# Optimization experiments

Hardware: AMD Instinct MI355X
Metric: run time of the kernel (lower is better)

## Reference

```python
import jax, jax.numpy as jnp
import numpy as np

B, N, K = 32, 511, 2          # trees per batch, nodes per tree (full binary), max children
IN_DIM, MEM_DIM = 256, 256


def _build_children_idx():
    # Heap tree (node p has children 2p+1, 2p+2), relabeled i -> N-1-i so that every
    # child id < parent id; then a single pass i = 0..N-1 is a valid topological order
    # (leaves first, root last at index N-1). Padded child slots are -1.
    ch = np.full((N, K), -1, dtype=np.int64)
    for p in range(N):
        for k in range(K):
            c = 2 * p + 1 + k
            if c < N:
                ch[N - 1 - p, k] = N - 1 - c
    return jnp.asarray(ch)


def setup_inputs() -> dict:
    key = jax.random.key(0)
    ks = jax.random.split(key, 9)
    s_in = float(1.0 / np.sqrt(IN_DIM))   # torch Linear default init bound
    s_m = float(1.0 / np.sqrt(MEM_DIM))
    u = lambda k, shape, s: jax.random.uniform(k, shape, jnp.float32, -s, s)
    return {
        "inputs": jax.random.normal(ks[0], (B, N, IN_DIM), jnp.float32),
        "W_ioux": u(ks[1], (3 * MEM_DIM, IN_DIM), s_in),
        "b_ioux": u(ks[2], (3 * MEM_DIM,), s_in),
        "W_iouh": u(ks[3], (3 * MEM_DIM, MEM_DIM), s_m),
        "b_iouh": u(ks[4], (3 * MEM_DIM,), s_m),
        "W_fx": u(ks[5], (MEM_DIM, IN_DIM), s_in),
        "b_fx": u(ks[6], (MEM_DIM,), s_in),
        "W_fh": u(ks[7], (MEM_DIM, MEM_DIM), s_m),
        "b_fh": u(ks[8], (MEM_DIM,), s_m),
        "children_idx": _build_children_idx(),
    }


def reference(inputs, W_ioux, b_ioux, W_iouh, b_iouh, W_fx, b_fx, W_fh, b_fh,
              children_idx):
    # Input-only projections depend on no recurrent state -> one big GEMM up front.
    x_iou = jnp.einsum('bni,oi->nbo', inputs, W_ioux) + b_ioux   # [N,B,3M]
    x_f = jnp.einsum('bni,mi->nbm', inputs, W_fx) + b_fx          # [N,B,M]

    def step(carry, xs):
        c_buf, h_buf, idx = carry                  # [N,B,M], [N,B,M], scalar node id
        ch, xi, xf = xs                            # [K], [B,3M], [B,M]
        valid = ch >= 0
        mask = valid.astype(c_buf.dtype)[:, None, None]
        safe = jnp.where(valid, ch, 0)
        child_c = c_buf[safe] * mask               # [K,B,M] (zeros for padded / leaf)
        child_h = h_buf[safe] * mask               # [K,B,M]
        h_sum = child_h.sum(0)                     # [B,M]  (child-sum)
        iou = xi + h_sum @ W_iouh.T + b_iouh       # [B,3M]
        i, o, u = jnp.split(iou, 3, axis=-1)
        i, o, u = jax.nn.sigmoid(i), jax.nn.sigmoid(o), jnp.tanh(u)
        # per-child forget gate: fh(child_h) + fx(inputs) broadcast over children
        f = jax.nn.sigmoid(jnp.einsum('kbm,nm->kbn', child_h, W_fh) + b_fh + xf[None])
        c = i * u + (f * child_c).sum(0)           # [B,M]
        h = o * jnp.tanh(c)
        c_buf = c_buf.at[idx].set(c)
        h_buf = h_buf.at[idx].set(h)
        return (c_buf, h_buf, idx + 1), None

    zeros = jnp.zeros((N, B, MEM_DIM), inputs.dtype)
    (c_buf, h_buf, _), _ = jax.lax.scan(
        step, (zeros, zeros, jnp.int32(0)), (children_idx, x_iou, x_f))

    root_c = c_buf[N - 1]                # [B,M]
    root_h = h_buf[N - 1]                # [B,M]
    hiddens = h_buf.transpose(1, 0, 2)   # [B,N,M]: h of node i at row i (tree.idx == i)
    return root_c, root_h, hiddens
```

## Files before the change

kernel.cpp:

```cpp
#include <hip/hip_runtime.h>
#include <hip/hip_bf16.h>


#define NN 511
#define BB 32
#define DD 256

typedef __attribute__((ext_vector_type(8))) short short8;
typedef __attribute__((ext_vector_type(4))) short short4v;
typedef __attribute__((ext_vector_type(4))) float f32x4;

#define MFMA __builtin_amdgcn_mfma_f32_16x16x32_bf16

#define OFF_XBF   0UL
#define OFF_HBF   8372224UL
#define OFF_CBUF  16744448UL
#define OFF_PART  33488896UL
#define OFF_WX    66912256UL
#define OFF_WH    67436544UL
#define OFF_BIAS  67960832UL

__device__ __forceinline__ short f2bf(float f) {
    union { float f; unsigned int u; } v; v.f = f;
    unsigned int r = (v.u + 0x7FFFu + ((v.u >> 16) & 1u)) >> 16;
    return (short)(unsigned short)r;
}
__device__ __forceinline__ float sigmf(float x) { return 1.0f / (1.0f + __expf(-x)); }
__device__ __forceinline__ float tanhc(float x) {
    x = fminf(fmaxf(x, -15.f), 15.f);
    float e = __expf(2.f * x);
    return (e - 1.f) / (e + 1.f);
}

__global__ void prep_x(const float* __restrict__ inp, short* __restrict__ xbf) {
    int idx = blockIdx.x * 256 + threadIdx.x;
    if (idx >= NN * BB * 64) return;
    int n = idx / (BB * 64);
    int rem = idx - n * (BB * 64);
    int b = rem >> 6;
    int c4 = rem & 63;
    float4 v = ((const float4*)(inp + ((long)b * NN + n) * DD))[c4];
    short4v sv = { f2bf(v.x), f2bf(v.y), f2bf(v.z), f2bf(v.w) };
    *(short4v*)(xbf + (long)idx * 4) = sv;
}

__global__ void prep_w(const float* __restrict__ Wix, const float* __restrict__ Wih,
                       const float* __restrict__ Wfx, const float* __restrict__ Wfh,
                       const float* __restrict__ bix, const float* __restrict__ bih,
                       const float* __restrict__ bfx, const float* __restrict__ bfh,
                       short* __restrict__ wx, short* __restrict__ wh,
                       float* __restrict__ bias) {
    int tid = blockIdx.x * 256 + threadIdx.x;
    if (tid >= 1024 * 256) return;
    int row = tid >> 8, c = tid & 255;
    float vx = (row < 768) ? Wix[row * 256 + c] : Wfx[(row - 768) * 256 + c];
    float vh = (row < 768) ? Wih[row * 256 + c] : Wfh[(row - 768) * 256 + c];
    wx[tid] = f2bf(vx);
    wh[tid] = f2bf(vh);
    if (c == 0)
        bias[row] = (row < 768) ? (bix[row] + bih[row]) : (bfx[row - 768] + bfh[row - 768]);
}

__device__ __forceinline__ void stage_w(const short* __restrict__ wsrc, int mt,
                                        short* __restrict__ lb, int tid) {
#pragma unroll
    for (int it = 0; it < 8; ++it) {
        const int u = it * 256 + tid;
        const int s = u >> 9;
        const int r = (u >> 5) & 15;
        const int c8 = u & 31;
        const int k = c8 * 8;
        short8 v = *(const short8*)(wsrc + ((long)(s * 256 + mt * 16 + r) * 256 + k));
        *(short8*)(lb + (s * 16 + r) * 256 + (k ^ ((r & 7) << 3))) = v;
    }
}

__global__ __launch_bounds__(256, 4) void xproj(
    const short* __restrict__ xbf, const short* __restrict__ wx,
    const float* __restrict__ bias, short* __restrict__ hbf,
    float* __restrict__ cbuf, float* __restrict__ part, float* __restrict__ out) {
    __shared__ short lb[4 * 16 * 256];
    const int tid = threadIdx.x;
    const int mt = blockIdx.y;
    stage_w(wx, mt, lb, tid);
    __syncthreads();

    const int lane = tid & 63;
    const int wid = tid >> 6;
    const int rt = blockIdx.x * 4 + wid;
    if (rt >= 2 * NN) return;
    const int arow = lane & 15;
    const int kgrp = lane >> 4;
    const int node = rt >> 1;
    const int bh = rt & 1;
    const int m = mt * 16 + arow;
    const int swz = (arow & 7) << 3;

    const short* ap = xbf + ((long)rt * 16 + arow) * DD + kgrp * 8;
    short8 a[8];
#pragma unroll
    for (int ks = 0; ks < 8; ++ks) a[ks] = *(const short8*)(ap + ks * 32);

    f32x4 ai = {0.f, 0.f, 0.f, 0.f}, ao = ai, au = ai, af = ai;
    const short* b0 = lb + (0 * 16 + arow) * 256;
    const short* b1 = lb + (1 * 16 + arow) * 256;
    const short* b2 = lb + (2 * 16 + arow) * 256;
    const short* b3 = lb + (3 * 16 + arow) * 256;
#pragma unroll
    for (int ks = 0; ks < 8; ++ks) {
        const int ko = (ks * 32 + kgrp * 8) ^ swz;
        short8 wi = *(const short8*)(b0 + ko);
        short8 wo = *(const short8*)(b1 + ko);
        short8 wu = *(const short8*)(b2 + ko);
        short8 wf = *(const short8*)(b3 + ko);
        ai = MFMA(a[ks], wi, ai, 0, 0, 0);
        ao = MFMA(a[ks], wo, ao, 0, 0, 0);
        au = MFMA(a[ks], wu, au, 0, 0, 0);
        af = MFMA(a[ks], wf, af, 0, 0, 0);
    }

    if (node < 256) {
        const float bi = bias[m], bo = bias[256 + m], bu = bias[512 + m];
#pragma unroll
        for (int r = 0; r < 4; ++r) {
            const int b = bh * 16 + kgrp * 4 + r;
            const float iv = sigmf(ai[r] + bi);
            const float ov = sigmf(ao[r] + bo);
            const float uv = tanhc(au[r] + bu);
            const float c = iv * uv;
            const float h = ov * tanhc(c);
            const long rowg = (long)node * BB + b;
            cbuf[rowg * DD + m] = c;
            hbf[rowg * DD + m] = f2bf(h);
            out[2 * BB * DD + ((long)b * NN + node) * DD + m] = h;
        }
    } else {
        const float bi = bias[m], bo = bias[256 + m], bu = bias[512 + m], bf = bias[768 + m];
#pragma unroll
        for (int r = 0; r < 4; ++r) {
            const int b = bh * 16 + kgrp * 4 + r;
            const long prow = ((long)(node - 256) * BB + b) * 1024;
            part[prow + m] = ai[r] + bi;
            part[prow + 256 + m] = ao[r] + bo;
            part[prow + 512 + m] = au[r] + bu;
            part[prow + 768 + m] = af[r] + bf;
        }
    }
}

__global__ __launch_bounds__(256, 4) void level_h(
    const short* __restrict__ wh, short* __restrict__ hbf,
    float* __restrict__ cbuf, const float* __restrict__ part,
    float* __restrict__ out, int istart, int ncount) {
    __shared__ short lb[4 * 16 * 256];
    const int tid = threadIdx.x;
    const int mt = blockIdx.y;
    stage_w(wh, mt, lb, tid);
    __syncthreads();

    const int lane = tid & 63;
    const int wid = tid >> 6;
    const int rt = blockIdx.x * 4 + wid;
    if (rt >= ncount * 2) return;
    const int arow = lane & 15;
    const int kgrp = lane >> 4;
    const int node = istart + (rt >> 1);
    const int bh = rt & 1;
    const int m = mt * 16 + arow;
    const int swz = (arow & 7) << 3;
    const int c0 = 2 * node - 511, c1 = 2 * node - 512;

    const short* ap0 = hbf + ((long)c0 * BB + bh * 16 + arow) * DD + kgrp * 8;
    const short* ap1 = hbf + ((long)c1 * BB + bh * 16 + arow) * DD + kgrp * 8;
    short8 a0[8], a1[8];
#pragma unroll
    for (int ks = 0; ks < 8; ++ks) {
        a0[ks] = *(const short8*)(ap0 + ks * 32);
        a1[ks] = *(const short8*)(ap1 + ks * 32);
    }

    f32x4 ai = {0.f, 0.f, 0.f, 0.f}, ao = ai, au = ai, f0a = ai, f1a = ai;
    const short* b0 = lb + (0 * 16 + arow) * 256;
    const short* b1 = lb + (1 * 16 + arow) * 256;
    const short* b2 = lb + (2 * 16 + arow) * 256;
    const short* b3 = lb + (3 * 16 + arow) * 256;
#pragma unroll
    for (int ks = 0; ks < 8; ++ks) {
        const int ko = (ks * 32 + kgrp * 8) ^ swz;
        short8 wi = *(const short8*)(b0 + ko);
        short8 wo = *(const short8*)(b1 + ko);
        short8 wu = *(const short8*)(b2 + ko);
        short8 wf = *(const short8*)(b3 + ko);
        ai = MFMA(a0[ks], wi, ai, 0, 0, 0);
        ai = MFMA(a1[ks], wi, ai, 0, 0, 0);
        ao = MFMA(a0[ks], wo, ao, 0, 0, 0);
        ao = MFMA(a1[ks], wo, ao, 0, 0, 0);
        au = MFMA(a0[ks], wu, au, 0, 0, 0);
        au = MFMA(a1[ks], wu, au, 0, 0, 0);
        f0a = MFMA(a0[ks], wf, f0a, 0, 0, 0);
        f1a = MFMA(a1[ks], wf, f1a, 0, 0, 0);
    }

#pragma unroll
    for (int r = 0; r < 4; ++r) {
        const int b = bh * 16 + kgrp * 4 + r;
        const long prow = ((long)(node - 256) * BB + b) * 1024;
        const float iv = sigmf(ai[r] + part[prow + m]);
        const float ov = sigmf(ao[r] + part[prow + 256 + m]);
        const float uv = tanhc(au[r] + part[prow + 512 + m]);
        const float pf = part[prow + 768 + m];
        const float f0 = sigmf(f0a[r] + pf);
        const float f1 = sigmf(f1a[r] + pf);
        const float cc0 = cbuf[((long)c0 * BB + b) * DD + m];
        const float cc1 = cbuf[((long)c1 * BB + b) * DD + m];
        const float c = iv * uv + f0 * cc0 + f1 * cc1;
        const float h = ov * tanhc(c);
        const long rowg = (long)node * BB + b;
        cbuf[rowg * DD + m] = c;
        hbf[rowg * DD + m] = f2bf(h);
        out[2 * BB * DD + ((long)b * NN + node) * DD + m] = h;
        if (node == NN - 1) {
            out[b * DD + m] = c;
            out[BB * DD + b * DD + m] = h;
        }
    }
}

extern "C" void kernel_launch(void* const* d_in, const int* in_sizes, int n_in,
                              void* d_out, int out_size, void* d_ws, size_t ws_size,
                              hipStream_t stream) {
    (void)in_sizes; (void)n_in; (void)out_size; (void)ws_size;
    const float* inputs = (const float*)d_in[0];
    const float* W_ioux = (const float*)d_in[1];
    const float* b_ioux = (const float*)d_in[2];
    const float* W_iouh = (const float*)d_in[3];
    const float* b_iouh = (const float*)d_in[4];
    const float* W_fx = (const float*)d_in[5];
    const float* b_fx = (const float*)d_in[6];
    const float* W_fh = (const float*)d_in[7];
    const float* b_fh = (const float*)d_in[8];

    char* ws = (char*)d_ws;
    short* xbf = (short*)(ws + OFF_XBF);
    short* hbf = (short*)(ws + OFF_HBF);
    float* cbuf = (float*)(ws + OFF_CBUF);
    float* part = (float*)(ws + OFF_PART);
    short* wx = (short*)(ws + OFF_WX);
    short* wh = (short*)(ws + OFF_WH);
    float* bias = (float*)(ws + OFF_BIAS);
    float* outp = (float*)d_out;

    prep_x<<<dim3((NN * BB * 64 + 255) / 256), dim3(256), 0, stream>>>(inputs, xbf);
    prep_w<<<dim3(1024), dim3(256), 0, stream>>>(W_ioux, W_iouh, W_fx, W_fh,
                                                 b_ioux, b_iouh, b_fx, b_fh, wx, wh, bias);

    xproj<<<dim3((2 * NN + 3) / 4, 16), dim3(256), 0, stream>>>(
        xbf, wx, bias, hbf, cbuf, part, outp);

    for (int d = 7; d >= 0; --d) {
        const int istart = 512 - (1 << (d + 1));
        const int ncount = 1 << d;
        level_h<<<dim3((ncount * 2 + 3) / 4, 16), dim3(256), 0, stream>>>(
            wh, hbf, cbuf, part, outp, istart, ncount);
    }
}
```

Measured before the change: 99.66 us.

## Fuse internal-node input projection into level kernels, drop fp32 partial buffer

The x-projection for internal nodes moves out of the up-front xproj kernel and into each level_h kernel, which now multiplies both the node's input and its children's hidden states against a concatenated [W_x|W_h] bf16 weight held in shared memory. This removes writing and then reading back the 32MB fp32 partial-gate buffer. In exchange each level kernel stages twice the weights into LDS (64KB, with launch bounds lowered to 2 blocks per SM) and does extra MFMA work on the serial level chain.

```diff
diff --git a/kernel.cpp b/kernel.cpp
--- a/kernel.cpp
+++ b/kernel.cpp
@@ -15,10 +15,8 @@
 #define OFF_XBF   0UL
 #define OFF_HBF   8372224UL
 #define OFF_CBUF  16744448UL
-#define OFF_PART  33488896UL
-#define OFF_WX    66912256UL
-#define OFF_WH    67436544UL
-#define OFF_BIAS  67960832UL
+#define OFF_WCAT  33488896UL
+#define OFF_BIAS  34537472UL
 
 __device__ __forceinline__ short f2bf(float f) {
     union { float f; unsigned int u; } v; v.f = f;
@@ -48,47 +46,41 @@
                        const float* __restrict__ Wfx, const float* __restrict__ Wfh,
                        const float* __restrict__ bix, const float* __restrict__ bih,
                        const float* __restrict__ bfx, const float* __restrict__ bfh,
-                       short* __restrict__ wx, short* __restrict__ wh,
-                       float* __restrict__ bias) {
+                       short* __restrict__ wcat, float* __restrict__ bias) {
     int tid = blockIdx.x * 256 + threadIdx.x;
-    if (tid >= 1024 * 256) return;
-    int row = tid >> 8, c = tid & 255;
-    float vx = (row < 768) ? Wix[row * 256 + c] : Wfx[(row - 768) * 256 + c];
-    float vh = (row < 768) ? Wih[row * 256 + c] : Wfh[(row - 768) * 256 + c];
-    wx[tid] = f2bf(vx);
-    wh[tid] = f2bf(vh);
+    if (tid >= 1024 * 512) return;
+    int row = tid >> 9, c = tid & 511;
+    float v;
+    if (c < 256) v = (row < 768) ? Wix[row * 256 + c] : Wfx[(row - 768) * 256 + c];
+    else         v = (row < 768) ? Wih[row * 256 + (c - 256)] : Wfh[(row - 768) * 256 + (c - 256)];
+    wcat[tid] = f2bf(v);
     if (c == 0)
         bias[row] = (row < 768) ? (bix[row] + bih[row]) : (bfx[row - 768] + bfh[row - 768]);
 }
 
-__device__ __forceinline__ void stage_w(const short* __restrict__ wsrc, int mt,
-                                        short* __restrict__ lb, int tid) {
+
+__global__ __launch_bounds__(256, 4) void xproj(
+    const short* __restrict__ xbf, const short* __restrict__ wcat,
+    const float* __restrict__ bias, short* __restrict__ hbf,
+    float* __restrict__ cbuf, float* __restrict__ out) {
+    __shared__ short lb[4 * 16 * 256];
+    const int tid = threadIdx.x;
+    const int mt = blockIdx.y;
 #pragma unroll
     for (int it = 0; it < 8; ++it) {
         const int u = it * 256 + tid;
         const int s = u >> 9;
         const int r = (u >> 5) & 15;
-        const int c8 = u & 31;
-        const int k = c8 * 8;
-        short8 v = *(const short8*)(wsrc + ((long)(s * 256 + mt * 16 + r) * 256 + k));
+        const int k = (u & 31) * 8;
+        short8 v = *(const short8*)(wcat + ((long)(s * 256 + mt * 16 + r) * 512 + k));
         *(short8*)(lb + (s * 16 + r) * 256 + (k ^ ((r & 7) << 3))) = v;
     }
-}
-
-__global__ __launch_bounds__(256, 4) void xproj(
-    const short* __restrict__ xbf, const short* __restrict__ wx,
-    const float* __restrict__ bias, short* __restrict__ hbf,
-    float* __restrict__ cbuf, float* __restrict__ part, float* __restrict__ out) {
-    __shared__ short lb[4 * 16 * 256];
-    const int tid = threadIdx.x;
-    const int mt = blockIdx.y;
-    stage_w(wx, mt, lb, tid);
     __syncthreads();
 
     const int lane = tid & 63;
     const int wid = tid >> 6;
     const int rt = blockIdx.x * 4 + wid;
-    if (rt >= 2 * NN) return;
+    if (rt >= 512) return;
     const int arow = lane & 15;
     const int kgrp = lane >> 4;
     const int node = rt >> 1;
@@ -101,67 +93,56 @@
 #pragma unroll
     for (int ks = 0; ks < 8; ++ks) a[ks] = *(const short8*)(ap + ks * 32);
 
-    f32x4 ai = {0.f, 0.f, 0.f, 0.f}, ao = ai, au = ai, af = ai;
+    f32x4 ai = {0.f, 0.f, 0.f, 0.f}, ao = ai, au = ai;
     const short* b0 = lb + (0 * 16 + arow) * 256;
     const short* b1 = lb + (1 * 16 + arow) * 256;
     const short* b2 = lb + (2 * 16 + arow) * 256;
-    const short* b3 = lb + (3 * 16 + arow) * 256;
 #pragma unroll
     for (int ks = 0; ks < 8; ++ks) {
         const int ko = (ks * 32 + kgrp * 8) ^ swz;
-        short8 wi = *(const short8*)(b0 + ko);
-        short8 wo = *(const short8*)(b1 + ko);
-        short8 wu = *(const short8*)(b2 + ko);
-        short8 wf = *(const short8*)(b3 + ko);
-        ai = MFMA(a[ks], wi, ai, 0, 0, 0);
-        ao = MFMA(a[ks], wo, ao, 0, 0, 0);
-        au = MFMA(a[ks], wu, au, 0, 0, 0);
-        af = MFMA(a[ks], wf, af, 0, 0, 0);
-    }
-
-    if (node < 256) {
-        const float bi = bias[m], bo = bias[256 + m], bu = bias[512 + m];
-#pragma unroll
-        for (int r = 0; r < 4; ++r) {
-            const int b = bh * 16 + kgrp * 4 + r;
-            const float iv = sigmf(ai[r] + bi);
-            const float ov = sigmf(ao[r] + bo);
-            const float uv = tanhc(au[r] + bu);
-            const float c = iv * uv;
-            const float h = ov * tanhc(c);
-            const long rowg = (long)node * BB + b;
-            cbuf[rowg * DD + m] = c;
-            hbf[rowg * DD + m] = f2bf(h);
-            out[2 * BB * DD + ((long)b * NN + node) * DD + m] = h;
-        }
-    } else {
-        const float bi = bias[m], bo = bias[256 + m], bu = bias[512 + m], bf = bias[768 + m];
-#pragma unroll
-        for (int r = 0; r < 4; ++r) {
-            const int b = bh * 16 + kgrp * 4 + r;
-            const long prow = ((long)(node - 256) * BB + b) * 1024;
-            part[prow + m] = ai[r] + bi;
-            part[prow + 256 + m] = ao[r] + bo;
-            part[prow + 512 + m] = au[r] + bu;
-            part[prow + 768 + m] = af[r] + bf;
-        }
-    }
-}
-
-__global__ __launch_bounds__(256, 4) void level_h(
-    const short* __restrict__ wh, short* __restrict__ hbf,
-    float* __restrict__ cbuf, const float* __restrict__ part,
-    float* __restrict__ out, int istart, int ncount) {
-    __shared__ short lb[4 * 16 * 256];
+        ai = MFMA(a[ks], *(const short8*)(b0 + ko), ai, 0, 0, 0);
+        ao = MFMA(a[ks], *(const short8*)(b1 + ko), ao, 0, 0, 0);
+        au = MFMA(a[ks], *(const short8*)(b2 + ko), au, 0, 0, 0);
+    }
+
+    const float bi = bias[m], bo = bias[256 + m], bu = bias[512 + m];
+#pragma unroll
+    for (int r = 0; r < 4; ++r) {
+        const int b = bh * 16 + kgrp * 4 + r;
+        const float iv = sigmf(ai[r] + bi);
+        const float ov = sigmf(ao[r] + bo);
+        const float uv = tanhc(au[r] + bu);
+        const float c = iv * uv;
+        const float h = ov * tanhc(c);
+        const long rowg = (long)node * BB + b;
+        cbuf[rowg * DD + m] = c;
+        hbf[rowg * DD + m] = f2bf(h);
+        out[2 * BB * DD + ((long)b * NN + node) * DD + m] = h;
+    }
+}
+
+__global__ __launch_bounds__(256, 2) void level_h(
+    const short* __restrict__ xbf, const short* __restrict__ wcat,
+    const float* __restrict__ bias, short* __restrict__ hbf,
+    float* __restrict__ cbuf, float* __restrict__ out, int istart, int ntasks) {
+    __shared__ short lb[4 * 16 * 512];
     const int tid = threadIdx.x;
     const int mt = blockIdx.y;
-    stage_w(wh, mt, lb, tid);
+#pragma unroll
+    for (int it = 0; it < 16; ++it) {
+        const int u = it * 256 + tid;
+        const int s = u >> 10;
+        const int r = (u >> 6) & 15;
+        const int k = (u & 63) * 8;
+        short8 v = *(const short8*)(wcat + ((long)(s * 256 + mt * 16 + r) * 512 + k));
+        *(short8*)(lb + (s * 16 + r) * 512 + (k ^ ((r & 7) << 3))) = v;
+    }
     __syncthreads();
 
     const int lane = tid & 63;
     const int wid = tid >> 6;
     const int rt = blockIdx.x * 4 + wid;
-    if (rt >= ncount * 2) return;
+    if (rt >= ntasks) return;
     const int arow = lane & 15;
     const int kgrp = lane >> 4;
     const int node = istart + (rt >> 1);
@@ -170,47 +151,63 @@
     const int swz = (arow & 7) << 3;
     const int c0 = 2 * node - 511, c1 = 2 * node - 512;
 
-    const short* ap0 = hbf + ((long)c0 * BB + bh * 16 + arow) * DD + kgrp * 8;
-    const short* ap1 = hbf + ((long)c1 * BB + bh * 16 + arow) * DD + kgrp * 8;
-    short8 a0[8], a1[8];
-#pragma unroll
-    for (int ks = 0; ks < 8; ++ks) {
-        a0[ks] = *(const short8*)(ap0 + ks * 32);
-        a1[ks] = *(const short8*)(ap1 + ks * 32);
-    }
-
-    f32x4 ai = {0.f, 0.f, 0.f, 0.f}, ao = ai, au = ai, f0a = ai, f1a = ai;
-    const short* b0 = lb + (0 * 16 + arow) * 256;
-    const short* b1 = lb + (1 * 16 + arow) * 256;
-    const short* b2 = lb + (2 * 16 + arow) * 256;
-    const short* b3 = lb + (3 * 16 + arow) * 256;
-#pragma unroll
-    for (int ks = 0; ks < 8; ++ks) {
-        const int ko = (ks * 32 + kgrp * 8) ^ swz;
-        short8 wi = *(const short8*)(b0 + ko);
-        short8 wo = *(const short8*)(b1 + ko);
-        short8 wu = *(const short8*)(b2 + ko);
-        short8 wf = *(const short8*)(b3 + ko);
-        ai = MFMA(a0[ks], wi, ai, 0, 0, 0);
-        ai = MFMA(a1[ks], wi, ai, 0, 0, 0);
-        ao = MFMA(a0[ks], wo, ao, 0, 0, 0);
-        ao = MFMA(a1[ks], wo, ao, 0, 0, 0);
-        au = MFMA(a0[ks], wu, au, 0, 0, 0);
-        au = MFMA(a1[ks], wu, au, 0, 0, 0);
-        f0a = MFMA(a0[ks], wf, f0a, 0, 0, 0);
-        f1a = MFMA(a1[ks], wf, f1a, 0, 0, 0);
-    }
-
+    const short* b0 = lb + (0 * 16 + arow) * 512;
+    const short* b1 = lb + (1 * 16 + arow) * 512;
+    const short* b2 = lb + (2 * 16 + arow) * 512;
+    const short* b3 = lb + (3 * 16 + arow) * 512;
+
+    f32x4 ai = {0.f, 0.f, 0.f, 0.f}, ao = ai, au = ai, afx = ai, af0 = ai, af1 = ai;
+
+    {
+        const short* ap = xbf + ((long)(node * BB + bh * 16) + arow) * DD + kgrp * 8;
+        short8 a[8];
+#pragma unroll
+        for (int ks = 0; ks < 8; ++ks) a[ks] = *(const short8*)(ap + ks * 32);
+#pragma unroll
+        for (int ks = 0; ks < 8; ++ks) {
+            const int ko = (ks * 32 + kgrp * 8) ^ swz;
+            ai = MFMA(a[ks], *(const short8*)(b0 + ko), ai, 0, 0, 0);
+            ao = MFMA(a[ks], *(const short8*)(b1 + ko), ao, 0, 0, 0);
+            au = MFMA(a[ks], *(const short8*)(b2 + ko), au, 0, 0, 0);
+            afx = MFMA(a[ks], *(const short8*)(b3 + ko), afx, 0, 0, 0);
+        }
+    }
+    {
+        const short* ap0 = hbf + ((long)(c0 * BB + bh * 16) + arow) * DD + kgrp * 8;
+        const short* ap1 = hbf + ((long)(c1 * BB + bh * 16) + arow) * DD + kgrp * 8;
+        short8 a0[8], a1[8];
+#pragma unroll
+        for (int ks = 0; ks < 8; ++ks) {
+            a0[ks] = *(const short8*)(ap0 + ks * 32);
+            a1[ks] = *(const short8*)(ap1 + ks * 32);
+        }
+#pragma unroll
+        for (int ks = 0; ks < 8; ++ks) {
+            const int ko = 256 + ((ks * 32 + kgrp * 8) ^ swz);
+            short8 wi = *(const short8*)(b0 + ko);
+            short8 wo = *(const short8*)(b1 + ko);
+            short8 wu = *(const short8*)(b2 + ko);
+            short8 wf = *(const short8*)(b3 + ko);
+            ai = MFMA(a0[ks], wi, ai, 0, 0, 0);
+            ai = MFMA(a1[ks], wi, ai, 0, 0, 0);
+            ao = MFMA(a0[ks], wo, ao, 0, 0, 0);
+            ao = MFMA(a1[ks], wo, ao, 0, 0, 0);
+            au = MFMA(a0[ks], wu, au, 0, 0, 0);
+            au = MFMA(a1[ks], wu, au, 0, 0, 0);
+            af0 = MFMA(a0[ks], wf, af0, 0, 0, 0);
+            af1 = MFMA(a1[ks], wf, af1, 0, 0, 0);
+        }
+    }
+
+    const float bi = bias[m], bo = bias[256 + m], bu = bias[512 + m], bf = bias[768 + m];
 #pragma unroll
     for (int r = 0; r < 4; ++r) {
         const int b = bh * 16 + kgrp * 4 + r;
-        const long prow = ((long)(node - 256) * BB + b) * 1024;
-        const float iv = sigmf(ai[r] + part[prow + m]);
-        const float ov = sigmf(ao[r] + part[prow + 256 + m]);
-        const float uv = tanhc(au[r] + part[prow + 512 + m]);
-        const float pf = part[prow + 768 + m];
-        const float f0 = sigmf(f0a[r] + pf);
-        const float f1 = sigmf(f1a[r] + pf);
+        const float iv = sigmf(ai[r] + bi);
+        const float ov = sigmf(ao[r] + bo);
+        const float uv = tanhc(au[r] + bu);
+        const float f0 = sigmf(afx[r] + af0[r] + bf);
+        const float f1 = sigmf(afx[r] + af1[r] + bf);
         const float cc0 = cbuf[((long)c0 * BB + b) * DD + m];
         const float cc1 = cbuf[((long)c1 * BB + b) * DD + m];
         const float c = iv * uv + f0 * cc0 + f1 * cc1;
@@ -244,23 +241,20 @@
     short* xbf = (short*)(ws + OFF_XBF);
     short* hbf = (short*)(ws + OFF_HBF);
     float* cbuf = (float*)(ws + OFF_CBUF);
-    float* part = (float*)(ws + OFF_PART);
-    short* wx = (short*)(ws + OFF_WX);
-    short* wh = (short*)(ws + OFF_WH);
+    short* wcat = (short*)(ws + OFF_WCAT);
     float* bias = (float*)(ws + OFF_BIAS);
     float* outp = (float*)d_out;
 
     prep_x<<<dim3((NN * BB * 64 + 255) / 256), dim3(256), 0, stream>>>(inputs, xbf);
-    prep_w<<<dim3(1024), dim3(256), 0, stream>>>(W_ioux, W_iouh, W_fx, W_fh,
-                                                 b_ioux, b_iouh, b_fx, b_fh, wx, wh, bias);
-
-    xproj<<<dim3((2 * NN + 3) / 4, 16), dim3(256), 0, stream>>>(
-        xbf, wx, bias, hbf, cbuf, part, outp);
+    prep_w<<<dim3(1024 * 512 / 256), dim3(256), 0, stream>>>(
+        W_ioux, W_iouh, W_fx, W_fh, b_ioux, b_iouh, b_fx, b_fh, wcat, bias);
+
+    xproj<<<dim3(128, 16), dim3(256), 0, stream>>>(xbf, wcat, bias, hbf, cbuf, outp);
 
     for (int d = 7; d >= 0; --d) {
         const int istart = 512 - (1 << (d + 1));
-        const int ncount = 1 << d;
-        level_h<<<dim3((ncount * 2 + 3) / 4, 16), dim3(256), 0, stream>>>(
-            wh, hbf, cbuf, part, outp, istart, ncount);
-    }
-}
+        const int ntasks = (1 << d) * 2;
+        level_h<<<dim3((ntasks + 3) / 4, 16), dim3(256), 0, stream>>>(
+            xbf, wcat, bias, hbf, cbuf, outp, istart, ntasks);
+    }
+}
```

After: 102.0 us. 2.4% more time.
